# Performance work log

Measured on AMD Instinct MI355X. Metric: run time of the kernel, lower is better.

Reference implementation:

```python
import jax, jax.numpy as jnp
import numpy as np
import math

N_HEADS = 4
N_ITERS = 2  # SSFormer n=2; each loop iteration recomputes the same values (no feedback in the original code)
BN_EPS = 1e-5


def _attention(q, k, v):
    """SSTransformer: multi-head cross-attention over flattened spatial dims.
    q,k,v: [B, C, H, W] -> returns [B, C, L] with L = H*W.
    """
    b, c = q.shape[0], q.shape[1]
    L = q.shape[2] * q.shape[3]
    ch = c // N_HEADS
    scale = 1.0 / math.sqrt(math.sqrt(ch))
    qf = (q.reshape(b * N_HEADS, ch, L) * scale)
    kf = (k.reshape(b * N_HEADS, ch, L) * scale)
    vf = v.reshape(b * N_HEADS, ch, L)
    # weight: [B*H, t, s]
    w = jnp.einsum('bct,bcs->bts', qf, kf)
    w = jax.nn.softmax(w.astype(jnp.float32), axis=-1).astype(w.dtype)
    a = jnp.einsum('bts,bcs->bct', w, vf)
    return a.reshape(b, c, L)


def setup_inputs() -> dict:
    key = jax.random.key(0)
    k1, k2, k3, k4 = jax.random.split(key, 4)
    B, C, H, W = 8, 512, 32, 32
    c = jax.random.normal(k1, (B, C, H, W), dtype=jnp.float32)
    e = jax.random.normal(k2, (B, C, H, W), dtype=jnp.float32)
    conv_w = jax.random.normal(k3, (C, C, 1, 1), dtype=jnp.float32) / math.sqrt(C)
    conv_b = jax.random.normal(k4, (C,), dtype=jnp.float32) * 0.02
    bn_gamma = jnp.ones((C,), dtype=jnp.float32)
    bn_beta = jnp.zeros((C,), dtype=jnp.float32)
    return {"c": c, "e": e, "conv_w": conv_w, "conv_b": conv_b,
            "bn_gamma": bn_gamma, "bn_beta": bn_beta}


def reference(c, e, conv_w, conv_b, bn_gamma, bn_beta):
    bs, ch, h, w = c.shape
    L = h * w
    for _ in range(N_ITERS):
        _c = _attention(e, c, c)                       # [B, C, L]
        _e = _attention(_c.reshape(bs, ch, h, w), e, e)  # [B, C, L]
    _e = _e.reshape(bs, ch, h, w)
    # Proj: 1x1 conv + BatchNorm2d (training-mode batch stats) + Swish
    x = jnp.einsum('oc,bchw->bohw', conv_w.reshape(ch, ch), _e) + conv_b[None, :, None, None]
    mean = jnp.mean(x, axis=(0, 2, 3), keepdims=True)
    var = jnp.var(x, axis=(0, 2, 3), keepdims=True)
    xn = (x - mean) * jax.lax.rsqrt(var + BN_EPS)
    xn = xn * bn_gamma[None, :, None, None] + bn_beta[None, :, None, None]
    return xn * jax.nn.sigmoid(xn)
```

## Files before the change

kernel.cpp:

```cpp
#include <hip/hip_runtime.h>
#include <hip/hip_bf16.h>

typedef __attribute__((ext_vector_type(8))) short short8;
typedef __attribute__((ext_vector_type(4))) float floatx4;
typedef __attribute__((ext_vector_type(4))) float f32x4;
typedef __attribute__((ext_vector_type(16))) float f32x16;
typedef unsigned short u16;
typedef unsigned int u32;
typedef __attribute__((ext_vector_type(4))) unsigned int u32x4;
typedef __attribute__((ext_vector_type(8))) unsigned short ushort8;

#define LSEQ 1024
#define CHD  128
#define CEXP 0.12751744900425577f
#define THR_RAW 62.73318f

static __device__ __forceinline__ float b2f(u16 u) {
  union { u32 i; float f; } x; x.i = ((u32)u) << 16; return x.f;
}
static __device__ __forceinline__ u16 f2b(float f) {
  __hip_bfloat16 h = __float2bfloat16(f);
  return *reinterpret_cast<u16*>(&h);
}
static __device__ __forceinline__ u32 cvtpk(float a, float b) {
  u32 r;
  asm("v_cvt_pk_bf16_f32 %0, %1, %2" : "=v"(r) : "v"(a), "v"(b));
  return r;
}
static __device__ __forceinline__ void swap32(u32& a, u32& b) {
  asm("v_permlane32_swap_b32 %0, %1" : "+v"(a), "+v"(b));
}
static __device__ __forceinline__ short8 mk8(u32 a, u32 b, u32 c, u32 d) {
  union { u32x4 u; short8 s; } x;
  x.u[0] = a; x.u[1] = b; x.u[2] = c; x.u[3] = d;
  return x.s;
}
static __device__ __forceinline__ float exp2f_fast(float x) {
  float r;
  asm("v_exp_f32 %0, %1" : "=v"(r) : "v"(x));
  return r;
}
static __device__ __forceinline__ void gl_lds16(const void* g, void* l) {
  __builtin_amdgcn_global_load_lds((__attribute__((address_space(1))) const void*)g,
                                   (__attribute__((address_space(3))) void*)l, 16, 0, 0);
}
#define BARRIER() do { asm volatile("" ::: "memory"); __builtin_amdgcn_s_barrier(); asm volatile("" ::: "memory"); } while (0)
#define LGKM0()   do { asm volatile("s_waitcnt lgkmcnt(0)" ::: "memory"); __builtin_amdgcn_sched_barrier(0); } while (0)

__global__ __launch_bounds__(256) void k_prep(const float* __restrict__ cin,
                                              const float* __restrict__ ein,
                                              const float* __restrict__ Wf,
                                              u16* __restrict__ cV, u16* __restrict__ cT,
                                              u16* __restrict__ eV, u16* __restrict__ eT,
                                              u16* __restrict__ wb) {
  __shared__ u16 tile[32][72];
  int z = blockIdx.z;
  int tid = threadIdx.x;
  if (z >= 64) {
    int wblk = (z - 64) * 64 + blockIdx.y * 16 + blockIdx.x;
    int base = (wblk * 256 + tid) * 8;
    f32x4 a = *(const f32x4*)(Wf + base);
    f32x4 b = *(const f32x4*)(Wf + base + 4);
    u32x4 u;
    u[0] = cvtpk(a[0], a[1]); u[1] = cvtpk(a[2], a[3]);
    u[2] = cvtpk(b[0], b[1]); u[3] = cvtpk(b[2], b[3]);
    *(u32x4*)(wb + base) = u;
    return;
  }
  const float* in = (z < 32) ? cin : ein;
  u16* outV = (z < 32) ? cV : eV;
  u16* outT = (z < 32) ? cT : eT;
  int bh = z & 31, c0 = blockIdx.y * 32, s0 = blockIdx.x * 64;
  int cl = tid >> 3, sc = tid & 7;
  size_t off = ((size_t)bh * CHD + c0 + cl) * LSEQ + s0 + sc * 8;
  f32x4 a = *(const f32x4*)(in + off);
  f32x4 b = *(const f32x4*)(in + off + 4);
  u32x4 u;
  u[0] = cvtpk(a[0], a[1]); u[1] = cvtpk(a[2], a[3]);
  u[2] = cvtpk(b[0], b[1]); u[3] = cvtpk(b[2], b[3]);
  *(u32x4*)(outV + off) = u;
  *(u32x4*)&tile[cl][sc * 8] = u;
  __syncthreads();
  int sl = tid >> 2, cc = tid & 3;
  ushort8 v;
#pragma unroll
  for (int j = 0; j < 8; ++j) v[j] = tile[cc * 8 + j][sl];
  *(ushort8*)(outT + ((size_t)bh * LSEQ + s0 + sl) * CHD + c0 + cc * 8) = v;
}

__global__ __launch_bounds__(256, 2) void k_attn(const u16* __restrict__ eT,
                                                 const u16* __restrict__ cT,
                                                 const u16* __restrict__ cV,
                                                 const u16* __restrict__ eV,
                                                 u16* __restrict__ outT) {
  __shared__ char ldsbuf[66560];

  int bh = blockIdx.x, tt = blockIdx.y;
  int tid = threadIdx.x;
  int w = tid >> 6, lane = tid & 63;
  int tw = w & 1, sw = w >> 1;
  int ln = lane & 31, h = lane >> 5;
  int t0 = tt * 64 + tw * 32;

  float* bmbuf = (float*)(ldsbuf + 65536);
  float* lbuf  = (float*)(ldsbuf + 65536 + 512);

  auto stageK = [&](int buf, int sb, const char* kTb) {
#pragma unroll
    for (int it = 0; it < 4; ++it) {
      int bb = it * 4096 + tid * 16;
      int row = bb >> 8;
      int cb = (bb & 255) ^ ((row & 15) << 4);
      gl_lds16(kTb + (size_t)(sb * 64 + row) * 256 + cb, ldsbuf + buf * 16384 + bb);
    }
  };
  auto stageV = [&](int buf, int sb, const char* vb) {
#pragma unroll
    for (int it = 0; it < 4; ++it) {
      int bb = it * 4096 + tid * 16;
      int row = bb >> 7;
      int cb = (bb & 127) ^ ((row & 7) << 4);
      gl_lds16(vb + (size_t)row * 2048 + sb * 128 + cb, ldsbuf + 32768 + buf * 16384 + bb);
    }
  };

  short8 bq[8];
  f32x16 oacc[4];
  float m_r, l_r;
  int swz = (ln & 7) << 4;
  int kswz = (ln & 15) << 4;
  int krow = sw * 32 + ln;

  auto flash = [&](const char* kTb, const char* vb) {
    m_r = -1e30f; l_r = 0.f;
#pragma unroll
    for (int i = 0; i < 4; ++i)
#pragma unroll
      for (int r = 0; r < 16; ++r) oacc[i][r] = 0.f;

    stageK(0, 0, kTb); stageV(0, 0, vb);
    asm volatile("s_waitcnt vmcnt(0)" ::: "memory");
    BARRIER();

    for (int sb = 0; sb < 16; ++sb) {
      int cur = sb & 1;
      const char* K = ldsbuf + cur * 16384;
      const char* V = ldsbuf + 32768 + cur * 16384;
      f32x16 sa;
#pragma unroll
      for (int r = 0; r < 16; ++r) sa[r] = 0.f;

      if (sb < 15) stageK(cur ^ 1, sb + 1, kTb);
      short8 ka0 = *(const short8*)(K + krow * 256 + ((0  + h * 16) ^ kswz));
      short8 ka1 = *(const short8*)(K + krow * 256 + ((32 + h * 16) ^ kswz));
      short8 ka2 = *(const short8*)(K + krow * 256 + ((64 + h * 16) ^ kswz));
      short8 ka3 = *(const short8*)(K + krow * 256 + ((96 + h * 16) ^ kswz));
      BARRIER();
      LGKM0();
      __builtin_amdgcn_s_setprio(1);
      sa = __builtin_amdgcn_mfma_f32_32x32x16_bf16(ka0, bq[0], sa, 0, 0, 0);
      sa = __builtin_amdgcn_mfma_f32_32x32x16_bf16(ka1, bq[1], sa, 0, 0, 0);
      sa = __builtin_amdgcn_mfma_f32_32x32x16_bf16(ka2, bq[2], sa, 0, 0, 0);
      sa = __builtin_amdgcn_mfma_f32_32x32x16_bf16(ka3, bq[3], sa, 0, 0, 0);
      __builtin_amdgcn_s_setprio(0);
      BARRIER();

      if (sb < 15) stageV(cur ^ 1, sb + 1, vb);
      short8 kb0 = *(const short8*)(K + krow * 256 + ((128 + h * 16) ^ kswz));
      short8 kb1 = *(const short8*)(K + krow * 256 + ((160 + h * 16) ^ kswz));
      short8 kb2 = *(const short8*)(K + krow * 256 + ((192 + h * 16) ^ kswz));
      short8 kb3 = *(const short8*)(K + krow * 256 + ((224 + h * 16) ^ kswz));
      BARRIER();
      LGKM0();
      __builtin_amdgcn_s_setprio(1);
      sa = __builtin_amdgcn_mfma_f32_32x32x16_bf16(kb0, bq[4], sa, 0, 0, 0);
      sa = __builtin_amdgcn_mfma_f32_32x32x16_bf16(kb1, bq[5], sa, 0, 0, 0);
      sa = __builtin_amdgcn_mfma_f32_32x32x16_bf16(kb2, bq[6], sa, 0, 0, 0);
      sa = __builtin_amdgcn_mfma_f32_32x32x16_bf16(kb3, bq[7], sa, 0, 0, 0);
      __builtin_amdgcn_s_setprio(0);
      BARRIER();

      float bm = fmaxf(fmaxf(sa[0], sa[1]), fmaxf(sa[2], sa[3]));
      bm = fmaxf(bm, fmaxf(fmaxf(sa[4], sa[5]), fmaxf(sa[6], sa[7])));
      bm = fmaxf(bm, fmaxf(fmaxf(sa[8], sa[9]), fmaxf(sa[10], sa[11])));
      bm = fmaxf(bm, fmaxf(fmaxf(sa[12], sa[13]), fmaxf(sa[14], sa[15])));
      bm = fmaxf(bm, __shfl_xor(bm, 32));
      if (lane < 32) bmbuf[(tw * 2 + sw) * 32 + lane] = bm;
      LGKM0();
      BARRIER();
      bm = fmaxf(bm, bmbuf[(tw * 2 + (sw ^ 1)) * 32 + ln]);
      bool stay = __all(bm - m_r <= THR_RAW);
      if (!stay) {
        float mn = fmaxf(m_r, bm);
        float corr = exp2f_fast((m_r - mn) * CEXP);
        m_r = mn; l_r *= corr;
#pragma unroll
        for (int i = 0; i < 4; ++i)
#pragma unroll
          for (int r = 0; r < 16; ++r) oacc[i][r] *= corr;
      }
      float mnC = m_r * CEXP;
      float rs = 0.f;
#pragma unroll
      for (int r = 0; r < 16; ++r) {
        float p = exp2f_fast(__builtin_fmaf(sa[r], CEXP, -mnC));
        sa[r] = p; rs += p;
      }
      rs += __shfl_xor(rs, 32);
      l_r += rs;

      short8 bp0, bp1;
      {
        u32 w0 = cvtpk(sa[0], sa[1]),  w1 = cvtpk(sa[2], sa[3]);
        u32 w2 = cvtpk(sa[4], sa[5]),  w3 = cvtpk(sa[6], sa[7]);
        swap32(w0, w2); swap32(w1, w3);
        bp0 = mk8(w0, w1, w2, w3);
        u32 w4 = cvtpk(sa[8], sa[9]),  w5 = cvtpk(sa[10], sa[11]);
        u32 w6 = cvtpk(sa[12], sa[13]), w7 = cvtpk(sa[14], sa[15]);
        swap32(w4, w6); swap32(w5, w7);
        bp1 = mk8(w4, w5, w6, w7);
      }

      int vc0 = sw * 64 + h * 16;
      short8 va0 = *(const short8*)(V + (0  + ln) * 128 + (vc0 ^ swz));
      short8 va1 = *(const short8*)(V + (32 + ln) * 128 + (vc0 ^ swz));
      short8 va2 = *(const short8*)(V + (64 + ln) * 128 + (vc0 ^ swz));
      short8 va3 = *(const short8*)(V + (96 + ln) * 128 + (vc0 ^ swz));
      BARRIER();
      LGKM0();
      __builtin_amdgcn_s_setprio(1);
      oacc[0] = __builtin_amdgcn_mfma_f32_32x32x16_bf16(va0, bp0, oacc[0], 0, 0, 0);
      oacc[1] = __builtin_amdgcn_mfma_f32_32x32x16_bf16(va1, bp0, oacc[1], 0, 0, 0);
      oacc[2] = __builtin_amdgcn_mfma_f32_32x32x16_bf16(va2, bp0, oacc[2], 0, 0, 0);
      oacc[3] = __builtin_amdgcn_mfma_f32_32x32x16_bf16(va3, bp0, oacc[3], 0, 0, 0);
      __builtin_amdgcn_s_setprio(0);
      BARRIER();

      int vc1 = sw * 64 + 32 + h * 16;
      short8 vb0 = *(const short8*)(V + (0  + ln) * 128 + (vc1 ^ swz));
      short8 vb1 = *(const short8*)(V + (32 + ln) * 128 + (vc1 ^ swz));
      short8 vb2 = *(const short8*)(V + (64 + ln) * 128 + (vc1 ^ swz));
      short8 vb3 = *(const short8*)(V + (96 + ln) * 128 + (vc1 ^ swz));
      BARRIER();
      LGKM0();
      __builtin_amdgcn_s_setprio(1);
      oacc[0] = __builtin_amdgcn_mfma_f32_32x32x16_bf16(vb0, bp1, oacc[0], 0, 0, 0);
      oacc[1] = __builtin_amdgcn_mfma_f32_32x32x16_bf16(vb1, bp1, oacc[1], 0, 0, 0);
      oacc[2] = __builtin_amdgcn_mfma_f32_32x32x16_bf16(vb2, bp1, oacc[2], 0, 0, 0);
      oacc[3] = __builtin_amdgcn_mfma_f32_32x32x16_bf16(vb3, bp1, oacc[3], 0, 0, 0);
      __builtin_amdgcn_s_setprio(0);
      asm volatile("s_waitcnt vmcnt(0)" ::: "memory");
      BARRIER();
    }
  };

  auto merge_sw = [&]() {
    float* mb = (float*)(ldsbuf + 32768 + tw * 16384);
    if (sw == 1) {
#pragma unroll
      for (int i = 0; i < 4; ++i)
#pragma unroll
        for (int r = 0; r < 16; ++r) mb[(i * 16 + r) * 64 + lane] = oacc[i][r];
      if (lane < 32) lbuf[tw * 32 + lane] = l_r;
    }
    LGKM0();
    BARRIER();
    if (sw == 0) {
#pragma unroll
      for (int i = 0; i < 4; ++i)
#pragma unroll
        for (int r = 0; r < 16; ++r) oacc[i][r] += mb[(i * 16 + r) * 64 + lane];
      l_r += lbuf[tw * 32 + ln];
    }
  };

  const u16* qbase = eT + ((size_t)bh * LSEQ + t0 + ln) * CHD + h * 8;
#pragma unroll
  for (int k = 0; k < 8; ++k) bq[k] = *(const short8*)(qbase + k * 16);

  flash((const char*)(cT + (size_t)bh * LSEQ * CHD),
        (const char*)(cV + (size_t)bh * CHD * LSEQ));

  merge_sw();
  if (sw == 0) {
    float inv = 1.0f / l_r;
    char* qt = ldsbuf + tw * 8192;
#pragma unroll
    for (int m = 0; m < 4; ++m)
#pragma unroll
      for (int q = 0; q < 8; ++q) {
        u32 pk = cvtpk(oacc[m][2 * q] * inv, oacc[m][2 * q + 1] * inv);
        int c2 = m * 64 + 4 * (q & 1) + 16 * (q >> 1) + 8 * h;
        *(u32*)(qt + ln * 256 + (c2 ^ swz)) = pk;
      }
  }
  LGKM0();
  BARRIER();
  {
    const char* qt = ldsbuf + tw * 8192;
#pragma unroll
    for (int k = 0; k < 8; ++k)
      bq[k] = *(const short8*)(qt + ln * 256 + ((k * 32 + h * 16) ^ swz));
  }
  LGKM0();
  BARRIER();

  flash((const char*)(eT + (size_t)bh * LSEQ * CHD),
        (const char*)(eV + (size_t)bh * CHD * LSEQ));

  merge_sw();
  BARRIER();
  if (sw == 0) {
    float inv = 1.0f / l_r;
    char* ot = ldsbuf + tw * 8192;
#pragma unroll
    for (int m = 0; m < 4; ++m)
#pragma unroll
      for (int q = 0; q < 8; ++q) {
        u32 pk = cvtpk(oacc[m][2 * q] * inv, oacc[m][2 * q + 1] * inv);
        int c2 = m * 64 + 4 * (q & 1) + 16 * (q >> 1) + 8 * h;
        *(u32*)(ot + ln * 256 + (c2 ^ swz)) = pk;
      }
    asm volatile("" ::: "memory");
    u16* orow = outT + ((size_t)bh * LSEQ + t0 + ln) * CHD;
#pragma unroll
    for (int it = 0; it < 8; ++it) {
      int col = h * 128 + it * 16;
      ushort8 d = *(const ushort8*)(ot + ln * 256 + (col ^ swz));
      *(ushort8*)((char*)orow + col) = d;
    }
  }
}

__global__ __launch_bounds__(256) void k_proj(const u16* __restrict__ Wm,
                                              const u16* __restrict__ eT,
                                              const float* __restrict__ bias,
                                              u16* __restrict__ x,
                                              float* __restrict__ pstat) {
  __shared__ char lds[65536];
  int lt = blockIdx.x, ot = blockIdx.y;
  int b = lt >> 3;
  int l0b = (lt & 7) * 128;
  int o0 = ot * 128;
  int tid = threadIdx.x, w = tid >> 6, lane = tid & 63, lo = lane & 15, hi = lane >> 4;
  int wm = w >> 1, wn = w & 1;
  const char* Wb = (const char*)Wm;
  const char* eTb = (const char*)eT;

  auto stageA = [&](int buf, int kb) {
    char* dst = lds + buf * 16384;
#pragma unroll
    for (int it = 0; it < 4; ++it) {
      int bb = it * 4096 + tid * 16;
      int row = bb >> 7;
      int cb = (bb & 127) ^ ((row & 7) << 4);
      gl_lds16(Wb + (size_t)(o0 + row) * 1024 + kb * 128 + cb, dst + bb);
    }
  };
  auto stageB = [&](int buf, int kb) {
    char* dst = lds + 32768 + buf * 16384;
    int page = b * 4 + (kb >> 1);
    int choff = (kb & 1) * 128;
#pragma unroll
    for (int it = 0; it < 4; ++it) {
      int bb = it * 4096 + tid * 16;
      int row = bb >> 7;
      int cb = (bb & 127) ^ ((row & 7) << 4);
      gl_lds16(eTb + ((size_t)page * 1024 + l0b + row) * 256 + choff + cb, dst + bb);
    }
  };

  floatx4 acc[4][4];
#pragma unroll
  for (int i = 0; i < 4; ++i)
#pragma unroll
    for (int j = 0; j < 4; ++j) { acc[i][j][0]=0.f; acc[i][j][1]=0.f; acc[i][j][2]=0.f; acc[i][j][3]=0.f; }

  stageA(0, 0); stageB(0, 0);

  for (int kb = 0; kb < 8; ++kb) {
    int cur = kb & 1;
    __builtin_amdgcn_s_barrier();
    if (kb < 7) { stageA(cur ^ 1, kb + 1); stageB(cur ^ 1, kb + 1); }
    if (kb < 7) { asm volatile("s_waitcnt vmcnt(8)" ::: "memory"); }
    else        { asm volatile("s_waitcnt vmcnt(0)" ::: "memory"); }
    __builtin_amdgcn_s_barrier();
    const char* A = lds + cur * 16384;
    const char* B = lds + 32768 + cur * 16384;
#pragma unroll
    for (int kk = 0; kk < 2; ++kk) {
      short8 af[4], bf[4];
#pragma unroll
      for (int mi = 0; mi < 4; ++mi) {
        int row = wm * 64 + mi * 16 + lo;
        af[mi] = *(const short8*)(A + row * 128 + ((kk * 64 + hi * 16) ^ ((row & 7) << 4)));
      }
#pragma unroll
      for (int ni = 0; ni < 4; ++ni) {
        int row = wn * 64 + ni * 16 + lo;
        bf[ni] = *(const short8*)(B + row * 128 + ((kk * 64 + hi * 16) ^ ((row & 7) << 4)));
      }
      __builtin_amdgcn_s_setprio(1);
#pragma unroll
      for (int mi = 0; mi < 4; ++mi)
#pragma unroll
        for (int ni = 0; ni < 4; ++ni)
          acc[mi][ni] = __builtin_amdgcn_mfma_f32_16x16x32_bf16(af[mi], bf[ni], acc[mi][ni], 0, 0, 0);
      __builtin_amdgcn_s_setprio(0);
    }
  }

  int prow = lt * 2 + wn;
#pragma unroll
  for (int mi = 0; mi < 4; ++mi) {
#pragma unroll
    for (int r = 0; r < 4; ++r) {
      int o = o0 + wm * 64 + mi * 16 + hi * 4 + r;
      float bv = bias[o];
      float s = 0.f, q = 0.f;
#pragma unroll
      for (int ni = 0; ni < 4; ++ni) {
        float xv = acc[mi][ni][r] + bv;
        x[((size_t)b * 512 + o) * LSEQ + l0b + wn * 64 + ni * 16 + lo] = f2b(xv);
        s += xv; q += xv * xv;
      }
#pragma unroll
      for (int d = 1; d < 16; d <<= 1) { s += __shfl_xor(s, d); q += __shfl_xor(q, d); }
      if (lo == 0) {
        pstat[(size_t)prow * 512 + o] = s;
        pstat[65536 + (size_t)prow * 512 + o] = q;
      }
    }
  }
}

__global__ __launch_bounds__(256) void k_stats(const float* __restrict__ pstat,
                                               const float* __restrict__ gamma,
                                               const float* __restrict__ beta,
                                               float* __restrict__ scale,
                                               float* __restrict__ shift) {
  int o = blockIdx.x * 256 + threadIdx.x;
  float s = 0.f, q = 0.f;
#pragma unroll 4
  for (int r = 0; r < 128; ++r) {
    s += pstat[(size_t)r * 512 + o];
    q += pstat[65536 + (size_t)r * 512 + o];
  }
  const float invn = 1.0f / 8192.0f;
  float mean = s * invn;
  float var = q * invn - mean * mean;
  float rstd = rsqrtf(var + 1e-5f);
  float g = gamma[o] * rstd;
  scale[o] = g;
  shift[o] = beta[o] - mean * g;
}

__global__ __launch_bounds__(256) void k_final(const u16* __restrict__ x,
                                               const float* __restrict__ scale,
                                               const float* __restrict__ shift,
                                               float* __restrict__ out) {
  int idx = blockIdx.x * 256 + threadIdx.x;
  int base = idx * 8;
  int ch = (base >> 10) & 511;
  float sc = scale[ch], sh = shift[ch];
  ushort8 vx = *(const ushort8*)(x + base);
  f32x4 o0, o1;
#pragma unroll
  for (int j = 0; j < 8; ++j) {
    float xn = b2f(vx[j]) * sc + sh;
    float sg = 1.0f / (1.0f + __expf(-xn));
    float r = xn * sg;
    if (j < 4) o0[j] = r; else o1[j - 4] = r;
  }
  *(f32x4*)(out + base) = o0;
  *(f32x4*)(out + base + 4) = o1;
}

extern "C" void kernel_launch(void* const* d_in, const int* in_sizes, int n_in,
                              void* d_out, int out_size, void* d_ws, size_t ws_size,
                              hipStream_t stream) {
  const float* c     = (const float*)d_in[0];
  const float* e     = (const float*)d_in[1];
  const float* Wf    = (const float*)d_in[2];
  const float* bias  = (const float*)d_in[3];
  const float* gamma = (const float*)d_in[4];
  const float* beta  = (const float*)d_in[5];
  float* outp = (float*)d_out;

  char* ws = (char*)d_ws;
  const size_t TB = (size_t)32 * 1024 * 128 * 2;
  u16* eT  = (u16*)(ws);
  u16* cT  = (u16*)(ws + TB);
  u16* cV  = (u16*)(ws + 2 * TB);
  u16* eV  = (u16*)(ws + 3 * TB);
  u16* xT  = (u16*)(ws + 4 * TB);
  u16* Wbf = (u16*)(ws + 5 * TB);
  float* scale = (float*)(ws + 5 * TB + (1 << 20));
  float* shift = scale + 512;
  float* pstat = (float*)(ws + 5 * TB + (2 << 20));
  u16* x   = (u16*)(ws + 6 * TB);

  dim3 tb(256);

  k_prep<<<dim3(16, 4, 66), tb, 0, stream>>>(c, e, Wf, cV, cT, eV, eT, Wbf);
  k_attn<<<dim3(32, 16), tb, 0, stream>>>(eT, cT, cV, eV, xT);
  k_proj<<<dim3(64, 4), tb, 0, stream>>>(Wbf, xT, bias, x, pstat);
  k_stats<<<dim3(2), tb, 0, stream>>>(pstat, gamma, beta, scale, shift);
  k_final<<<dim3(2048), tb, 0, stream>>>(x, scale, shift, outp);
}
```

Baseline: 102.6 us.

## Fuse projection, BN stats and Swish into one cooperative kernel with grid syncs

The projection GEMM, the batch-norm statistics reduction and the final normalize+Swish pass are merged into one kernel launched cooperatively. Accumulators stay in registers across two grid-wide barriers instead of writing a bf16 intermediate and reading it back. This removes two kernel launches and the round trip of the intermediate tensor through global memory. In exchange it adds two grid syncs, and the 256 blocks with 64KB LDS each must all be co-resident for the cooperative launch to succeed.

```diff
diff --git a/kernel.cpp b/kernel.cpp
--- a/kernel.cpp
+++ b/kernel.cpp
@@ -1,5 +1,8 @@
 #include <hip/hip_runtime.h>
 #include <hip/hip_bf16.h>
+#include <hip/hip_cooperative_groups.h>
+
+namespace cg = cooperative_groups;
 
 typedef __attribute__((ext_vector_type(8))) short short8;
 typedef __attribute__((ext_vector_type(4))) float floatx4;
@@ -17,10 +20,6 @@
 
 static __device__ __forceinline__ float b2f(u16 u) {
   union { u32 i; float f; } x; x.i = ((u32)u) << 16; return x.f;
-}
-static __device__ __forceinline__ u16 f2b(float f) {
-  __hip_bfloat16 h = __float2bfloat16(f);
-  return *reinterpret_cast<u16*>(&h);
 }
 static __device__ __forceinline__ u32 cvtpk(float a, float b) {
   u32 r;
@@ -332,11 +331,13 @@
   }
 }
 
-__global__ __launch_bounds__(256) void k_proj(const u16* __restrict__ Wm,
-                                              const u16* __restrict__ eT,
-                                              const float* __restrict__ bias,
-                                              u16* __restrict__ x,
-                                              float* __restrict__ pstat) {
+__global__ __launch_bounds__(256) void k_projfused(const u16* __restrict__ Wm,
+                                                   const u16* __restrict__ eT,
+                                                   const float* __restrict__ bias,
+                                                   float* __restrict__ pstat,
+                                                   const float* __restrict__ gamma,
+                                                   const float* __restrict__ beta,
+                                                   float* __restrict__ outp) {
   __shared__ char lds[65536];
   int lt = blockIdx.x, ot = blockIdx.y;
   int b = lt >> 3;
@@ -421,7 +422,7 @@
 #pragma unroll
       for (int ni = 0; ni < 4; ++ni) {
         float xv = acc[mi][ni][r] + bv;
-        x[((size_t)b * 512 + o) * LSEQ + l0b + wn * 64 + ni * 16 + lo] = f2b(xv);
+        acc[mi][ni][r] = xv;
         s += xv; q += xv * xv;
       }
 #pragma unroll
@@ -432,48 +433,48 @@
       }
     }
   }
-}
-
-__global__ __launch_bounds__(256) void k_stats(const float* __restrict__ pstat,
-                                               const float* __restrict__ gamma,
-                                               const float* __restrict__ beta,
-                                               float* __restrict__ scale,
-                                               float* __restrict__ shift) {
-  int o = blockIdx.x * 256 + threadIdx.x;
-  float s = 0.f, q = 0.f;
-#pragma unroll 4
-  for (int r = 0; r < 128; ++r) {
-    s += pstat[(size_t)r * 512 + o];
-    q += pstat[65536 + (size_t)r * 512 + o];
-  }
-  const float invn = 1.0f / 8192.0f;
-  float mean = s * invn;
-  float var = q * invn - mean * mean;
-  float rstd = rsqrtf(var + 1e-5f);
-  float g = gamma[o] * rstd;
-  scale[o] = g;
-  shift[o] = beta[o] - mean * g;
-}
-
-__global__ __launch_bounds__(256) void k_final(const u16* __restrict__ x,
-                                               const float* __restrict__ scale,
-                                               const float* __restrict__ shift,
-                                               float* __restrict__ out) {
-  int idx = blockIdx.x * 256 + threadIdx.x;
-  int base = idx * 8;
-  int ch = (base >> 10) & 511;
-  float sc = scale[ch], sh = shift[ch];
-  ushort8 vx = *(const ushort8*)(x + base);
-  f32x4 o0, o1;
-#pragma unroll
-  for (int j = 0; j < 8; ++j) {
-    float xn = b2f(vx[j]) * sc + sh;
-    float sg = 1.0f / (1.0f + __expf(-xn));
-    float r = xn * sg;
-    if (j < 4) o0[j] = r; else o1[j - 4] = r;
-  }
-  *(f32x4*)(out + base) = o0;
-  *(f32x4*)(out + base + 4) = o1;
+
+  __threadfence();
+  cg::this_grid().sync();
+
+  float* scale = pstat + 131072;
+  float* shift = scale + 512;
+  int bid = blockIdx.y * 64 + blockIdx.x;
+  if (tid < 128) {
+    int chn = bid * 2 + (tid >> 6);
+    int l = lane;
+    float s = pstat[(size_t)l * 512 + chn] + pstat[(size_t)(l + 64) * 512 + chn];
+    float q = pstat[65536 + (size_t)l * 512 + chn] + pstat[65536 + (size_t)(l + 64) * 512 + chn];
+#pragma unroll
+    for (int d = 1; d < 64; d <<= 1) { s += __shfl_xor(s, d); q += __shfl_xor(q, d); }
+    if (l == 0) {
+      const float invn = 1.0f / 8192.0f;
+      float mean = s * invn;
+      float var = q * invn - mean * mean;
+      float rstd = rsqrtf(var + 1e-5f);
+      float g = gamma[chn] * rstd;
+      scale[chn] = g;
+      shift[chn] = beta[chn] - mean * g;
+    }
+  }
+
+  __threadfence();
+  cg::this_grid().sync();
+
+#pragma unroll
+  for (int mi = 0; mi < 4; ++mi) {
+#pragma unroll
+    for (int r = 0; r < 4; ++r) {
+      int o = o0 + wm * 64 + mi * 16 + hi * 4 + r;
+      float sc = scale[o], sh = shift[o];
+#pragma unroll
+      for (int ni = 0; ni < 4; ++ni) {
+        float xn = acc[mi][ni][r] * sc + sh;
+        float sg = 1.0f / (1.0f + __expf(-xn));
+        outp[((size_t)b * 512 + o) * LSEQ + l0b + wn * 64 + ni * 16 + lo] = xn * sg;
+      }
+    }
+  }
 }
 
 extern "C" void kernel_launch(void* const* d_in, const int* in_sizes, int n_in,
@@ -495,16 +496,13 @@
   u16* eV  = (u16*)(ws + 3 * TB);
   u16* xT  = (u16*)(ws + 4 * TB);
   u16* Wbf = (u16*)(ws + 5 * TB);
-  float* scale = (float*)(ws + 5 * TB + (1 << 20));
-  float* shift = scale + 512;
   float* pstat = (float*)(ws + 5 * TB + (2 << 20));
-  u16* x   = (u16*)(ws + 6 * TB);
 
   dim3 tb(256);
 
   k_prep<<<dim3(16, 4, 66), tb, 0, stream>>>(c, e, Wf, cV, cT, eV, eT, Wbf);
   k_attn<<<dim3(32, 16), tb, 0, stream>>>(eT, cT, cV, eV, xT);
-  k_proj<<<dim3(64, 4), tb, 0, stream>>>(Wbf, xT, bias, x, pstat);
-  k_stats<<<dim3(2), tb, 0, stream>>>(pstat, gamma, beta, scale, shift);
-  k_final<<<dim3(2048), tb, 0, stream>>>(x, scale, shift, outp);
-}
+  void* args[] = { (void*)&Wbf, (void*)&xT, (void*)&bias, (void*)&pstat,
+                   (void*)&gamma, (void*)&beta, (void*)&outp };
+  hipLaunchCooperativeKernel((const void*)k_projfused, dim3(64, 4), tb, args, 0, stream);
+}
```

Measured after the change: 205.2 us. 2x slower.

## Fuse BN stats into final kernel and drop explicit LDS waits in flash loop

Applied to the files above, without the earlier changes.

Removes the separate k_stats launch: each k_final block now reduces the per-channel partial sums for its two channels with wave shuffles and keeps scale and shift in shared memory. It also removes the explicit lgkmcnt waits and sched_barriers before the MFMA groups in the attention loop, leaving the compiler to insert waits and schedule freely. The bf16 store in the projection switches to the packed convert instruction. This saves a launch and a serialization point, but every final block re-reads 256 stat values, and scheduling inside the attention loop may change unpredictably.

```diff
diff --git a/kernel.cpp b/kernel.cpp
--- a/kernel.cpp
+++ b/kernel.cpp
@@ -18,10 +18,6 @@
 static __device__ __forceinline__ float b2f(u16 u) {
   union { u32 i; float f; } x; x.i = ((u32)u) << 16; return x.f;
 }
-static __device__ __forceinline__ u16 f2b(float f) {
-  __hip_bfloat16 h = __float2bfloat16(f);
-  return *reinterpret_cast<u16*>(&h);
-}
 static __device__ __forceinline__ u32 cvtpk(float a, float b) {
   u32 r;
   asm("v_cvt_pk_bf16_f32 %0, %1, %2" : "=v"(r) : "v"(a), "v"(b));
@@ -45,7 +41,7 @@
                                    (__attribute__((address_space(3))) void*)l, 16, 0, 0);
 }
 #define BARRIER() do { asm volatile("" ::: "memory"); __builtin_amdgcn_s_barrier(); asm volatile("" ::: "memory"); } while (0)
-#define LGKM0()   do { asm volatile("s_waitcnt lgkmcnt(0)" ::: "memory"); __builtin_amdgcn_sched_barrier(0); } while (0)
+#define LGKMW()   do { asm volatile("s_waitcnt lgkmcnt(0)" ::: "memory"); } while (0)
 
 __global__ __launch_bounds__(256) void k_prep(const float* __restrict__ cin,
                                               const float* __restrict__ ein,
@@ -156,7 +152,6 @@
       short8 ka2 = *(const short8*)(K + krow * 256 + ((64 + h * 16) ^ kswz));
       short8 ka3 = *(const short8*)(K + krow * 256 + ((96 + h * 16) ^ kswz));
       BARRIER();
-      LGKM0();
       __builtin_amdgcn_s_setprio(1);
       sa = __builtin_amdgcn_mfma_f32_32x32x16_bf16(ka0, bq[0], sa, 0, 0, 0);
       sa = __builtin_amdgcn_mfma_f32_32x32x16_bf16(ka1, bq[1], sa, 0, 0, 0);
@@ -171,7 +166,6 @@
       short8 kb2 = *(const short8*)(K + krow * 256 + ((192 + h * 16) ^ kswz));
       short8 kb3 = *(const short8*)(K + krow * 256 + ((224 + h * 16) ^ kswz));
       BARRIER();
-      LGKM0();
       __builtin_amdgcn_s_setprio(1);
       sa = __builtin_amdgcn_mfma_f32_32x32x16_bf16(kb0, bq[4], sa, 0, 0, 0);
       sa = __builtin_amdgcn_mfma_f32_32x32x16_bf16(kb1, bq[5], sa, 0, 0, 0);
@@ -186,7 +180,7 @@
       bm = fmaxf(bm, fmaxf(fmaxf(sa[12], sa[13]), fmaxf(sa[14], sa[15])));
       bm = fmaxf(bm, __shfl_xor(bm, 32));
       if (lane < 32) bmbuf[(tw * 2 + sw) * 32 + lane] = bm;
-      LGKM0();
+      LGKMW();
       BARRIER();
       bm = fmaxf(bm, bmbuf[(tw * 2 + (sw ^ 1)) * 32 + ln]);
       bool stay = __all(bm - m_r <= THR_RAW);
@@ -227,7 +221,6 @@
       short8 va2 = *(const short8*)(V + (64 + ln) * 128 + (vc0 ^ swz));
       short8 va3 = *(const short8*)(V + (96 + ln) * 128 + (vc0 ^ swz));
       BARRIER();
-      LGKM0();
       __builtin_amdgcn_s_setprio(1);
       oacc[0] = __builtin_amdgcn_mfma_f32_32x32x16_bf16(va0, bp0, oacc[0], 0, 0, 0);
       oacc[1] = __builtin_amdgcn_mfma_f32_32x32x16_bf16(va1, bp0, oacc[1], 0, 0, 0);
@@ -242,7 +235,6 @@
       short8 vb2 = *(const short8*)(V + (64 + ln) * 128 + (vc1 ^ swz));
       short8 vb3 = *(const short8*)(V + (96 + ln) * 128 + (vc1 ^ swz));
       BARRIER();
-      LGKM0();
       __builtin_amdgcn_s_setprio(1);
       oacc[0] = __builtin_amdgcn_mfma_f32_32x32x16_bf16(vb0, bp1, oacc[0], 0, 0, 0);
       oacc[1] = __builtin_amdgcn_mfma_f32_32x32x16_bf16(vb1, bp1, oacc[1], 0, 0, 0);
@@ -263,7 +255,7 @@
         for (int r = 0; r < 16; ++r) mb[(i * 16 + r) * 64 + lane] = oacc[i][r];
       if (lane < 32) lbuf[tw * 32 + lane] = l_r;
     }
-    LGKM0();
+    LGKMW();
     BARRIER();
     if (sw == 0) {
 #pragma unroll
@@ -294,7 +286,7 @@
         *(u32*)(qt + ln * 256 + (c2 ^ swz)) = pk;
       }
   }
-  LGKM0();
+  LGKMW();
   BARRIER();
   {
     const char* qt = ldsbuf + tw * 8192;
@@ -302,7 +294,7 @@
     for (int k = 0; k < 8; ++k)
       bq[k] = *(const short8*)(qt + ln * 256 + ((k * 32 + h * 16) ^ swz));
   }
-  LGKM0();
+  LGKMW();
   BARRIER();
 
   flash((const char*)(eT + (size_t)bh * LSEQ * CHD),
@@ -421,7 +413,7 @@
 #pragma unroll
       for (int ni = 0; ni < 4; ++ni) {
         float xv = acc[mi][ni][r] + bv;
-        x[((size_t)b * 512 + o) * LSEQ + l0b + wn * 64 + ni * 16 + lo] = f2b(xv);
+        x[((size_t)b * 512 + o) * LSEQ + l0b + wn * 64 + ni * 16 + lo] = cvtpk(xv, xv) & 0xffff;
         s += xv; q += xv * xv;
       }
 #pragma unroll
@@ -434,35 +426,36 @@
   }
 }
 
-__global__ __launch_bounds__(256) void k_stats(const float* __restrict__ pstat,
+__global__ __launch_bounds__(256) void k_final(const u16* __restrict__ x,
+                                               const float* __restrict__ pstat,
                                                const float* __restrict__ gamma,
                                                const float* __restrict__ beta,
-                                               float* __restrict__ scale,
-                                               float* __restrict__ shift) {
-  int o = blockIdx.x * 256 + threadIdx.x;
-  float s = 0.f, q = 0.f;
-#pragma unroll 4
-  for (int r = 0; r < 128; ++r) {
-    s += pstat[(size_t)r * 512 + o];
-    q += pstat[65536 + (size_t)r * 512 + o];
-  }
-  const float invn = 1.0f / 8192.0f;
-  float mean = s * invn;
-  float var = q * invn - mean * mean;
-  float rstd = rsqrtf(var + 1e-5f);
-  float g = gamma[o] * rstd;
-  scale[o] = g;
-  shift[o] = beta[o] - mean * g;
-}
-
-__global__ __launch_bounds__(256) void k_final(const u16* __restrict__ x,
-                                               const float* __restrict__ scale,
-                                               const float* __restrict__ shift,
                                                float* __restrict__ out) {
-  int idx = blockIdx.x * 256 + threadIdx.x;
-  int base = idx * 8;
-  int ch = (base >> 10) & 511;
-  float sc = scale[ch], sh = shift[ch];
+  __shared__ float sscale[2], sshift[2];
+  int bid = blockIdx.x;
+  int tid = threadIdx.x;
+  if (tid < 128) {
+    int k = tid >> 6;
+    int chn = (bid * 2 + k) & 511;
+    int l = tid & 63;
+    float s = pstat[(size_t)l * 512 + chn] + pstat[(size_t)(l + 64) * 512 + chn];
+    float q = pstat[65536 + (size_t)l * 512 + chn] + pstat[65536 + (size_t)(l + 64) * 512 + chn];
+#pragma unroll
+    for (int d = 1; d < 64; d <<= 1) { s += __shfl_xor(s, d); q += __shfl_xor(q, d); }
+    if (l == 0) {
+      const float invn = 1.0f / 8192.0f;
+      float mean = s * invn;
+      float var = q * invn - mean * mean;
+      float rstd = rsqrtf(var + 1e-5f);
+      float g = gamma[chn] * rstd;
+      sscale[k] = g;
+      sshift[k] = beta[chn] - mean * g;
+    }
+  }
+  __syncthreads();
+  int base = (bid * 256 + tid) * 8;
+  int k2 = tid >> 7;
+  float sc = sscale[k2], sh = sshift[k2];
   ushort8 vx = *(const ushort8*)(x + base);
   f32x4 o0, o1;
 #pragma unroll
@@ -495,8 +488,6 @@
   u16* eV  = (u16*)(ws + 3 * TB);
   u16* xT  = (u16*)(ws + 4 * TB);
   u16* Wbf = (u16*)(ws + 5 * TB);
-  float* scale = (float*)(ws + 5 * TB + (1 << 20));
-  float* shift = scale + 512;
   float* pstat = (float*)(ws + 5 * TB + (2 << 20));
   u16* x   = (u16*)(ws + 6 * TB);
 
@@ -505,6 +496,5 @@
   k_prep<<<dim3(16, 4, 66), tb, 0, stream>>>(c, e, Wf, cV, cT, eV, eT, Wbf);
   k_attn<<<dim3(32, 16), tb, 0, stream>>>(eT, cT, cV, eV, xT);
   k_proj<<<dim3(64, 4), tb, 0, stream>>>(Wbf, xT, bias, x, pstat);
-  k_stats<<<dim3(2), tb, 0, stream>>>(pstat, gamma, beta, scale, shift);
-  k_final<<<dim3(2048), tb, 0, stream>>>(x, scale, shift, outp);
-}
+  k_final<<<dim3(2048), tb, 0, stream>>>(x, pstat, gamma, beta, outp);
+}
```

Result: faster. 93.38 us (median of 2 runs) (-9.0%).
